# Kernel tuning notes

Hardware: AMD Instinct MI355X
Metric: run time of the kernel (lower is better)

## Reference

```python
import jax, jax.numpy as jnp
import numpy as np

N_NODES = 200000
N_EDGES = 600000
EMB = 128
HID = 128
N_RELS = 64
N_MOTIFS = 512
N_CENTERS = 256
N_NODE_CLASSES = 16


def _linear_params(key, out_dim, in_dim):
    kw, kb = jax.random.split(key)
    s = 1.0 / np.sqrt(in_dim)
    w = jax.random.uniform(kw, (out_dim, in_dim), jnp.float32, -s, s)
    b = jax.random.uniform(kb, (out_dim,), jnp.float32, -s, s)
    return w, b


def setup_inputs() -> dict:
    key = jax.random.key(0)
    ks = jax.random.split(key, 12)
    lin_w, lin_b = _linear_params(ks[2], HID, EMB)
    conv1_w, conv1_b = _linear_params(ks[3], HID, HID)
    conv2_w, conv2_b = _linear_params(ks[4], HID, HID)
    edge_w, edge_b = _linear_params(ks[5], N_RELS, 2 * HID)
    motif_w, motif_b = _linear_params(ks[6], N_MOTIFS, HID)
    node_w, node_b = _linear_params(ks[7], N_NODE_CLASSES, HID)
    return {
        "node_emb": jax.random.normal(ks[0], (N_NODES, EMB), jnp.float32),
        "rel_emb": jax.random.normal(ks[1], (N_RELS, EMB), jnp.float32),
        "lin_w": lin_w, "lin_b": lin_b,
        "conv1_w": conv1_w, "conv1_b": conv1_b,
        "conv2_w": conv2_w, "conv2_b": conv2_b,
        "edge_w": edge_w, "edge_b": edge_b,
        "motif_w": motif_w, "motif_b": motif_b,
        "node_w": node_w, "node_b": node_b,
        "node_ids": jnp.arange(N_NODES, dtype=jnp.int32),
        "rel_ids": jax.random.randint(ks[8], (N_EDGES,), 0, N_RELS, jnp.int32),
        "center_mol_idx": jax.random.randint(ks[9], (N_CENTERS,), 0, N_NODES, jnp.int32),
        "edge_index": jax.random.randint(ks[10], (2, N_EDGES), 0, N_NODES, jnp.int32),
    }


def _gine_conv(x, edge_index, edge_attr, w, b):
    # PyG GINEConv (eps=0): nn((1+eps)*x + sum_j relu(x_j + e_ji))
    src, dst = edge_index[0], edge_index[1]
    msg = jax.nn.relu(x[src] + edge_attr)               # [E, H]
    agg = jax.ops.segment_sum(msg, dst, num_segments=x.shape[0])  # [N, H]
    return (agg + x) @ w.T + b


def reference(node_emb, rel_emb, lin_w, lin_b, conv1_w, conv1_b,
              conv2_w, conv2_b, edge_w, edge_b, motif_w, motif_b,
              node_w, node_b, node_ids, rel_ids, center_mol_idx, edge_index):
    x = node_emb[node_ids]            # [N, EMB]
    edge_attr = rel_emb[rel_ids]      # [E, EMB]
    x = x @ lin_w.T + lin_b           # [N, H]
    edge_attr = edge_attr @ lin_w.T + lin_b  # [E, H]
    x = _gine_conv(x, edge_index, edge_attr, conv1_w, conv1_b)
    x = jax.nn.relu(x)
    x = _gine_conv(x, edge_index, edge_attr, conv2_w, conv2_b)
    edge_pred_input = jnp.concatenate([x[edge_index[0]], x[edge_index[1]]], axis=1)  # [E, 2H]
    edge_class = edge_pred_input @ edge_w.T + edge_b       # [E, num_rels]
    center = x[center_mol_idx]                             # [C, H]
    motif_pred = center @ motif_w.T + motif_b              # [C, num_motifs]
    node_class = x @ node_w.T + node_b                     # [N, 16]
    return (edge_class, motif_pred, node_class)
```

## Files before the change

kernel.cpp:

```cpp
#include <hip/hip_runtime.h>
#include <hip/hip_bf16.h>

#define N_NODES 200000
#define N_EDGES 600000
#define EMB 128
#define HID 128
#define N_RELS 64
#define N_MOTIFS 512
#define N_CENTERS 256
#define NCLS 16

#define SCAN_C 512
#define NB_SCAN ((N_NODES + SCAN_C - 1) / SCAN_C)

typedef unsigned short u16;
typedef __attribute__((ext_vector_type(8))) short short8;
typedef __attribute__((ext_vector_type(4))) float f32x4;

__device__ __forceinline__ float bf2f(u16 u) {
    unsigned int i = ((unsigned int)u) << 16;
    float f; __builtin_memcpy(&f, &i, 4); return f;
}
__device__ __forceinline__ u16 f2bf(float f) {
    unsigned int x; __builtin_memcpy(&x, &f, 4);
    x += 0x7fffu + ((x >> 16) & 1u);
    return (u16)(x >> 16);
}

#define O_LINW   0
#define O_LINB   16384
#define O_C1W    16512
#define O_C1B    32896
#define O_C2W    33024
#define O_C2B    49408
#define O_EW     49536
#define O_EB     65920
#define O_MW     65984
#define O_MB     131520
#define O_NW     132032
#define O_NB     134080
#define N_WB     134096

__global__ void k_cvt(const float* __restrict__ lw, const float* __restrict__ lb,
                      const float* __restrict__ c1w, const float* __restrict__ c1b,
                      const float* __restrict__ c2w, const float* __restrict__ c2b,
                      const float* __restrict__ ew, const float* __restrict__ eb,
                      const float* __restrict__ mw, const float* __restrict__ mb,
                      const float* __restrict__ nw, const float* __restrict__ nb,
                      u16* __restrict__ wb)
{
    const int t = blockIdx.x * 256 + threadIdx.x;
    if (t >= N_WB) return;
    float v;
    if      (t < O_LINB) v = lw[t - O_LINW];
    else if (t < O_C1W)  v = lb[t - O_LINB];
    else if (t < O_C1B)  v = c1w[t - O_C1W];
    else if (t < O_C2W)  v = c1b[t - O_C1B];
    else if (t < O_C2B)  v = c2w[t - O_C2W];
    else if (t < O_EW)   v = c2b[t - O_C2B];
    else if (t < O_EB)   v = ew[t - O_EW];
    else if (t < O_MW)   v = eb[t - O_EB];
    else if (t < O_MB)   v = mw[t - O_MW];
    else if (t < O_NW)   v = mb[t - O_MB];
    else if (t < O_NB)   v = nw[t - O_NW];
    else                 v = nb[t - O_NB];
    wb[t] = f2bf(v);
}

__global__ void k_rel(const float* __restrict__ rel_emb, const float* __restrict__ lw,
                      const float* __restrict__ lb, float* __restrict__ rel_lin)
{
    __shared__ float e[EMB];
    const int r = blockIdx.x, h = threadIdx.x;
    e[h] = rel_emb[r * EMB + h];
    __syncthreads();
    const float* wr = lw + (size_t)h * EMB;
    float acc = lb[h];
    #pragma unroll
    for (int k0 = 0; k0 < EMB; k0 += 4) {
        f32x4 wv = *(const f32x4*)(wr + k0);
        #pragma unroll
        for (int j = 0; j < 4; ++j) acc += e[k0 + j] * wv[j];
    }
    rel_lin[r * HID + h] = acc;
}

__global__ void k_hist(const int* __restrict__ dst, int* __restrict__ deg)
{
    const int e = blockIdx.x * 256 + threadIdx.x;
    if (e < N_EDGES) atomicAdd(&deg[dst[e]], 1);
}

__global__ void k_scan1(const int* __restrict__ deg, int* __restrict__ bsum)
{
    __shared__ int sd[256];
    const int t = threadIdx.x, base = blockIdx.x * SCAN_C;
    int v = 0;
    int i0 = base + t, i1 = base + 256 + t;
    if (i0 < N_NODES) v += deg[i0];
    if (i1 < N_NODES) v += deg[i1];
    sd[t] = v; __syncthreads();
    for (int s = 128; s > 0; s >>= 1) {
        if (t < s) sd[t] += sd[t + s];
        __syncthreads();
    }
    if (t == 0) bsum[blockIdx.x] = sd[0];
}

__global__ void k_scan2(int* __restrict__ bsum, int* __restrict__ row_ptr)
{
    __shared__ int sh[512];
    const int t = threadIdx.x;
    int v = (t < NB_SCAN) ? bsum[t] : 0;
    sh[t] = v;
    for (int off = 1; off < 512; off <<= 1) {
        __syncthreads();
        int a = (t >= off) ? sh[t - off] : 0;
        __syncthreads();
        sh[t] += a;
    }
    __syncthreads();
    if (t < NB_SCAN) bsum[t] = sh[t] - v;
    if (t == 511) row_ptr[N_NODES] = sh[511];
}

__global__ void k_scan3(const int* __restrict__ deg, const int* __restrict__ bsum,
                        int* __restrict__ row_ptr)
{
    __shared__ int sh[256];
    const int t = threadIdx.x, base = blockIdx.x * SCAN_C;
    const int i0 = base + 2 * t, i1 = i0 + 1;
    int d0 = (i0 < N_NODES) ? deg[i0] : 0;
    int d1 = (i1 < N_NODES) ? deg[i1] : 0;
    int p = d0 + d1;
    sh[t] = p;
    for (int off = 1; off < 256; off <<= 1) {
        __syncthreads();
        int a = (t >= off) ? sh[t - off] : 0;
        __syncthreads();
        sh[t] += a;
    }
    __syncthreads();
    const int off = bsum[blockIdx.x] + sh[t] - p;
    if (i0 < N_NODES) row_ptr[i0] = off;
    if (i1 < N_NODES) row_ptr[i1] = off + d0;
}

__global__ void k_fill(const int* __restrict__ src, const int* __restrict__ dst,
                       const int* __restrict__ rid, const int* __restrict__ row_ptr,
                       int* __restrict__ cur, int* __restrict__ srcrid)
{
    const int e = blockIdx.x * 256 + threadIdx.x;
    if (e >= N_EDGES) return;
    const int d = dst[e];
    const int pos = row_ptr[d] + atomicAdd(&cur[d], 1);
    srcrid[pos] = src[e] * 64 + rid[e];
}

__global__ __launch_bounds__(256) void k_lin(
    const float* __restrict__ emb, const int* __restrict__ ids,
    const u16* __restrict__ w, const u16* __restrict__ bias,
    u16* __restrict__ out)
{
    const int wid = threadIdx.x >> 6, lane = threadIdx.x & 63;
    const int r15 = lane & 15, kg = (lane >> 4) * 8;
    const int arow = blockIdx.x * 64 + wid * 16 + r15;
    const int srow = ids[arow];
    const float* ar = emb + (size_t)srow * EMB + kg;
    short8 a[4];
    #pragma unroll
    for (int kk = 0; kk < 4; ++kk) {
        f32x4 a0 = *(const f32x4*)(ar + kk * 32);
        f32x4 a1 = *(const f32x4*)(ar + kk * 32 + 4);
        short8 t;
        #pragma unroll
        for (int j = 0; j < 4; ++j) { t[j] = (short)f2bf(a0[j]); t[4 + j] = (short)f2bf(a1[j]); }
        a[kk] = t;
    }
    f32x4 acc[8];
    #pragma unroll
    for (int nb = 0; nb < 8; ++nb) acc[nb] = (f32x4){0.f, 0.f, 0.f, 0.f};
    #pragma unroll
    for (int nb = 0; nb < 8; ++nb) {
        const u16* wr = w + (size_t)(nb * 16 + r15) * EMB + kg;
        #pragma unroll
        for (int kk = 0; kk < 4; ++kk) {
            short8 bv = *(const short8*)(wr + kk * 32);
            acc[nb] = __builtin_amdgcn_mfma_f32_16x16x32_bf16(a[kk], bv, acc[nb], 0, 0, 0);
        }
    }
    const int ob = blockIdx.x * 64 + wid * 16 + (lane >> 4) * 4;
    #pragma unroll
    for (int nb = 0; nb < 8; ++nb) {
        const int col = nb * 16 + r15;
        const float bn = bf2f(bias[col]);
        #pragma unroll
        for (int r = 0; r < 4; ++r)
            out[(size_t)(ob + r) * HID + col] = f2bf(acc[nb][r] + bn);
    }
}

#define RLD 132
#define ALD 136
__global__ __launch_bounds__(256) void k_fuse(
    const u16* __restrict__ x, const float* __restrict__ rel_lin,
    const int* __restrict__ row_ptr, const int* __restrict__ srcrid,
    const u16* __restrict__ w, const u16* __restrict__ bias,
    u16* __restrict__ out, const int do_relu)
{
    __shared__ float rel[N_RELS * RLD];
    __shared__ u16 atile[64 * ALD];
    {
        const int rr = threadIdx.x >> 2, qq = (threadIdx.x & 3) * 32;
        #pragma unroll
        for (int c = 0; c < 32; c += 4) {
            f32x4 v = *(const f32x4*)(rel_lin + rr * HID + qq + c);
            *(f32x4*)(&rel[rr * RLD + qq + c]) = v;
        }
    }
    __syncthreads();

    const int nl = threadIdx.x >> 2;
    const int n = blockIdx.x * 64 + nl;
    const int q = (threadIdx.x & 3) * 32;
    const int pbeg = row_ptr[n], pend = row_ptr[n + 1];

    float acc[32];
    #pragma unroll
    for (int j = 0; j < 32; ++j) acc[j] = 0.f;

    for (int p = pbeg; p < pend; ++p) {
        const int v = srcrid[p];
        const int s = v >> 6, r = v & 63;
        const u16* xp = x + (size_t)s * HID + q;
        const float* rp = &rel[r * RLD + q];
        #pragma unroll
        for (int c = 0; c < 4; ++c) {
            short8 xv = *(const short8*)(xp + c * 8);
            #pragma unroll
            for (int j = 0; j < 8; ++j)
                acc[c * 8 + j] += fmaxf(bf2f((u16)xv[j]) + rp[c * 8 + j], 0.f);
        }
    }
    {
        const u16* xp = x + (size_t)n * HID + q;
        #pragma unroll
        for (int c = 0; c < 4; ++c) {
            short8 xv = *(const short8*)(xp + c * 8);
            short8 t;
            #pragma unroll
            for (int j = 0; j < 8; ++j) t[j] = (short)f2bf(acc[c * 8 + j] + bf2f((u16)xv[j]));
            *(short8*)(&atile[nl * ALD + q + c * 8]) = t;
        }
    }
    __syncthreads();

    const int wid = threadIdx.x >> 6, lane = threadIdx.x & 63;
    const int r15 = lane & 15, kg = (lane >> 4) * 8;
    const int lrow = wid * 16 + r15;
    short8 a[4];
    #pragma unroll
    for (int kk = 0; kk < 4; ++kk) a[kk] = *(const short8*)(&atile[lrow * ALD + kg + kk * 32]);
    f32x4 accm[8];
    #pragma unroll
    for (int nb = 0; nb < 8; ++nb) accm[nb] = (f32x4){0.f, 0.f, 0.f, 0.f};
    #pragma unroll
    for (int nb = 0; nb < 8; ++nb) {
        const u16* wr = w + (size_t)(nb * 16 + r15) * HID + kg;
        #pragma unroll
        for (int kk = 0; kk < 4; ++kk) {
            short8 bv = *(const short8*)(wr + kk * 32);
            accm[nb] = __builtin_amdgcn_mfma_f32_16x16x32_bf16(a[kk], bv, accm[nb], 0, 0, 0);
        }
    }
    const int ob = blockIdx.x * 64 + wid * 16 + (lane >> 4) * 4;
    #pragma unroll
    for (int nb = 0; nb < 8; ++nb) {
        const int col = nb * 16 + r15;
        const float bn = bf2f(bias[col]);
        #pragma unroll
        for (int r = 0; r < 4; ++r) {
            float v = accm[nb][r] + bn;
            if (do_relu) v = fmaxf(v, 0.f);
            out[(size_t)(ob + r) * HID + col] = f2bf(v);
        }
    }
}

__global__ __launch_bounds__(256) void k_heads(
    const u16* __restrict__ x2, const u16* __restrict__ ew,
    const u16* __restrict__ nw, const u16* __restrict__ nbias,
    float* __restrict__ y, float* __restrict__ node_out)
{
    const int wid = threadIdx.x >> 6, lane = threadIdx.x & 63;
    const int r15 = lane & 15, kg = (lane >> 4) * 8;
    const int arow = blockIdx.x * 64 + wid * 16 + r15;
    const u16* xr = x2 + (size_t)arow * HID + kg;
    short8 a[4];
    #pragma unroll
    for (int kk = 0; kk < 4; ++kk) a[kk] = *(const short8*)(xr + kk * 32);

    f32x4 accs[4], accd[4], accn;
    #pragma unroll
    for (int nb = 0; nb < 4; ++nb) {
        accs[nb] = (f32x4){0.f, 0.f, 0.f, 0.f};
        accd[nb] = (f32x4){0.f, 0.f, 0.f, 0.f};
    }
    accn = (f32x4){0.f, 0.f, 0.f, 0.f};

    #pragma unroll
    for (int nb = 0; nb < 4; ++nb) {
        const u16* wr = ew + (size_t)(nb * 16 + r15) * 256 + kg;
        #pragma unroll
        for (int kk = 0; kk < 4; ++kk) {
            short8 bs = *(const short8*)(wr + kk * 32);
            short8 bd = *(const short8*)(wr + 128 + kk * 32);
            accs[nb] = __builtin_amdgcn_mfma_f32_16x16x32_bf16(a[kk], bs, accs[nb], 0, 0, 0);
            accd[nb] = __builtin_amdgcn_mfma_f32_16x16x32_bf16(a[kk], bd, accd[nb], 0, 0, 0);
        }
    }
    {
        const u16* wr = nw + (size_t)r15 * HID + kg;
        #pragma unroll
        for (int kk = 0; kk < 4; ++kk) {
            short8 bv = *(const short8*)(wr + kk * 32);
            accn = __builtin_amdgcn_mfma_f32_16x16x32_bf16(a[kk], bv, accn, 0, 0, 0);
        }
    }

    const int ob = blockIdx.x * 64 + wid * 16 + (lane >> 4) * 4;
    #pragma unroll
    for (int nb = 0; nb < 4; ++nb) {
        const int col = nb * 16 + r15;
        #pragma unroll
        for (int r = 0; r < 4; ++r) {
            y[(size_t)(ob + r) * 128 + col] = accs[nb][r];
            y[(size_t)(ob + r) * 128 + 64 + col] = accd[nb][r];
        }
    }
    const float bn = bf2f(nbias[r15]);
    #pragma unroll
    for (int r = 0; r < 4; ++r)
        node_out[(size_t)(ob + r) * NCLS + r15] = accn[r] + bn;
}

__global__ __launch_bounds__(256) void k_eout(
    const float* __restrict__ y, const int* __restrict__ src, const int* __restrict__ dst,
    const float* __restrict__ eb, float* __restrict__ out)
{
    const int t = blockIdx.x * 256 + threadIdx.x;
    const int e = t >> 2;
    const int qq = (t & 3) * 16;
    const int s = src[e], d = dst[e];
    const float* ys = y + (size_t)s * 128 + qq;
    const float* yd = y + (size_t)d * 128 + 64 + qq;
    const float* ebp = eb + qq;
    float* op = out + (size_t)e * 64 + qq;
    #pragma unroll
    for (int c = 0; c < 4; ++c) {
        f32x4 vs = *(const f32x4*)(ys + c * 4);
        f32x4 vd = *(const f32x4*)(yd + c * 4);
        f32x4 vb = *(const f32x4*)(ebp + c * 4);
        f32x4 r;
        #pragma unroll
        for (int j = 0; j < 4; ++j) r[j] = vs[j] + vd[j] + vb[j];
        *(f32x4*)(op + c * 4) = r;
    }
}

__global__ void k_motif(const u16* __restrict__ x2, const int* __restrict__ centers,
                        const u16* __restrict__ mw, const u16* __restrict__ mb,
                        float* __restrict__ out)
{
    __shared__ float xs[HID];
    const int c = blockIdx.x, m = threadIdx.x;
    if (m < HID) xs[m] = bf2f(x2[(size_t)centers[c] * HID + m]);
    __syncthreads();
    const u16* wr = mw + (size_t)m * HID;
    float acc = bf2f(mb[m]);
    #pragma unroll
    for (int k0 = 0; k0 < HID; k0 += 8) {
        short8 wv = *(const short8*)(wr + k0);
        #pragma unroll
        for (int j = 0; j < 8; ++j) acc += xs[k0 + j] * bf2f((u16)wv[j]);
    }
    out[(size_t)c * N_MOTIFS + m] = acc;
}

extern "C" void kernel_launch(void* const* d_in, const int* in_sizes, int n_in,
                              void* d_out, int out_size, void* d_ws, size_t ws_size,
                              hipStream_t stream)
{
    const float* node_emb = (const float*)d_in[0];
    const float* rel_emb  = (const float*)d_in[1];
    const float* lin_w    = (const float*)d_in[2];
    const float* lin_b    = (const float*)d_in[3];
    const float* conv1_w  = (const float*)d_in[4];
    const float* conv1_b  = (const float*)d_in[5];
    const float* conv2_w  = (const float*)d_in[6];
    const float* conv2_b  = (const float*)d_in[7];
    const float* edge_w   = (const float*)d_in[8];
    const float* edge_b   = (const float*)d_in[9];
    const float* motif_w  = (const float*)d_in[10];
    const float* motif_b  = (const float*)d_in[11];
    const float* node_w   = (const float*)d_in[12];
    const float* node_b   = (const float*)d_in[13];
    const int* node_ids = (const int*)d_in[14];
    const int* rel_ids  = (const int*)d_in[15];
    const int* centers  = (const int*)d_in[16];
    const int* src      = (const int*)d_in[17];
    const int* dst      = ((const int*)d_in[17]) + N_EDGES;

    char* ws = (char*)d_ws;
    float* rel_lin = (float*)ws;
    u16*   wb      = (u16*)(ws + 32768);
    u16*   x0      = (u16*)(ws + 524288);
    u16*   x1      = (u16*)(ws + 524288 + 51200000);
    float* y       = (float*)(ws + 524288 + 2 * 51200000);
    char*  csr     = ws + 524288 + 2 * 51200000 + 102400000;
    int*   deg     = (int*)csr;
    int*   cur     = (int*)(csr + 800000);
    int*   row_ptr = (int*)(csr + 1600000);
    int*   srcrid  = (int*)(csr + 2400032);
    int*   bsum    = (int*)(csr + 4800032);
    u16*   x2      = x0;

    float* out_edge  = (float*)d_out;
    float* out_motif = out_edge + (size_t)N_EDGES * 64;
    float* out_node  = out_motif + (size_t)N_CENTERS * N_MOTIFS;

    k_cvt<<<(N_WB + 255) / 256, 256, 0, stream>>>(
        lin_w, lin_b, conv1_w, conv1_b, conv2_w, conv2_b,
        edge_w, edge_b, motif_w, motif_b, node_w, node_b, wb);
    hipMemsetAsync(deg, 0, 1600000, stream);
    k_rel<<<N_RELS, 128, 0, stream>>>(rel_emb, lin_w, lin_b, rel_lin);

    k_hist<<<(N_EDGES + 255) / 256, 256, 0, stream>>>(dst, deg);
    k_scan1<<<NB_SCAN, 256, 0, stream>>>(deg, bsum);
    k_scan2<<<1, 512, 0, stream>>>(bsum, row_ptr);
    k_scan3<<<NB_SCAN, 256, 0, stream>>>(deg, bsum, row_ptr);
    k_fill<<<(N_EDGES + 255) / 256, 256, 0, stream>>>(src, dst, rel_ids, row_ptr, cur, srcrid);

    k_lin<<<N_NODES / 64, 256, 0, stream>>>(node_emb, node_ids, wb + O_LINW, wb + O_LINB, x0);
    k_fuse<<<N_NODES / 64, 256, 0, stream>>>(x0, rel_lin, row_ptr, srcrid,
                                             wb + O_C1W, wb + O_C1B, x1, 1);
    k_fuse<<<N_NODES / 64, 256, 0, stream>>>(x1, rel_lin, row_ptr, srcrid,
                                             wb + O_C2W, wb + O_C2B, x2, 0);
    k_heads<<<N_NODES / 64, 256, 0, stream>>>(x2, wb + O_EW, wb + O_NW, wb + O_NB, y, out_node);
    k_eout<<<(N_EDGES * 4) / 256, 256, 0, stream>>>(y, src, dst, edge_b, out_edge);
    k_motif<<<N_CENTERS, N_MOTIFS, 0, stream>>>(x2, centers, wb + O_MW, wb + O_MB, out_motif);
}
```

Before: 508.0 us.

## Read rel table from global, unroll edge loop by two, store head projections as bf16

The GINE aggregation kernel no longer stages the 64x128 fp32 relation table in shared memory. It reads the table straight from global memory/L1 and handles two edges per iteration so more gathers are in flight at once. This frees about 33KB of LDS per block, which should allow more blocks per CU. The per-node src/dst projections y are now stored as bf16 instead of fp32, halving the bytes the edge-output kernel gathers, at the cost of extra rounding in the edge logits.

New measurement: 541.0 us. 1.06x slower.

```diff
diff --git a/kernel.cpp b/kernel.cpp
--- a/kernel.cpp
+++ b/kernel.cpp
@@ -200,7 +200,6 @@
     }
 }
 
-#define RLD 132
 #define ALD 136
 __global__ __launch_bounds__(256) void k_fuse(
     const u16* __restrict__ x, const float* __restrict__ rel_lin,
@@ -208,17 +207,7 @@
     const u16* __restrict__ w, const u16* __restrict__ bias,
     u16* __restrict__ out, const int do_relu)
 {
-    __shared__ float rel[N_RELS * RLD];
     __shared__ u16 atile[64 * ALD];
-    {
-        const int rr = threadIdx.x >> 2, qq = (threadIdx.x & 3) * 32;
-        #pragma unroll
-        for (int c = 0; c < 32; c += 4) {
-            f32x4 v = *(const f32x4*)(rel_lin + rr * HID + qq + c);
-            *(f32x4*)(&rel[rr * RLD + qq + c]) = v;
-        }
-    }
-    __syncthreads();
 
     const int nl = threadIdx.x >> 2;
     const int n = blockIdx.x * 64 + nl;
@@ -229,11 +218,36 @@
     #pragma unroll
     for (int j = 0; j < 32; ++j) acc[j] = 0.f;
 
-    for (int p = pbeg; p < pend; ++p) {
+    int p = pbeg;
+    for (; p + 2 <= pend; p += 2) {
+        const int v0 = srcrid[p], v1 = srcrid[p + 1];
+        const int s0 = v0 >> 6, r0 = v0 & 63;
+        const int s1 = v1 >> 6, r1 = v1 & 63;
+        const u16* xp0 = x + (size_t)s0 * HID + q;
+        const u16* xp1 = x + (size_t)s1 * HID + q;
+        const float* rp0 = rel_lin + r0 * HID + q;
+        const float* rp1 = rel_lin + r1 * HID + q;
+        short8 xv0[4], xv1[4];
+        f32x4 rv0[8], rv1[8];
+        #pragma unroll
+        for (int c = 0; c < 4; ++c) { xv0[c] = *(const short8*)(xp0 + c * 8);
+                                      xv1[c] = *(const short8*)(xp1 + c * 8); }
+        #pragma unroll
+        for (int c = 0; c < 8; ++c) { rv0[c] = *(const f32x4*)(rp0 + c * 4);
+                                      rv1[c] = *(const f32x4*)(rp1 + c * 4); }
+        #pragma unroll
+        for (int c = 0; c < 4; ++c)
+            #pragma unroll
+            for (int j = 0; j < 8; ++j) {
+                acc[c * 8 + j] += fmaxf(bf2f((u16)xv0[c][j]) + rv0[c * 2 + (j >> 2)][j & 3], 0.f);
+                acc[c * 8 + j] += fmaxf(bf2f((u16)xv1[c][j]) + rv1[c * 2 + (j >> 2)][j & 3], 0.f);
+            }
+    }
+    if (p < pend) {
         const int v = srcrid[p];
         const int s = v >> 6, r = v & 63;
         const u16* xp = x + (size_t)s * HID + q;
-        const float* rp = &rel[r * RLD + q];
+        const float* rp = rel_lin + r * HID + q;
         #pragma unroll
         for (int c = 0; c < 4; ++c) {
             short8 xv = *(const short8*)(xp + c * 8);
@@ -290,7 +304,7 @@
 __global__ __launch_bounds__(256) void k_heads(
     const u16* __restrict__ x2, const u16* __restrict__ ew,
     const u16* __restrict__ nw, const u16* __restrict__ nbias,
-    float* __restrict__ y, float* __restrict__ node_out)
+    u16* __restrict__ y, float* __restrict__ node_out)
 {
     const int wid = threadIdx.x >> 6, lane = threadIdx.x & 63;
     const int r15 = lane & 15, kg = (lane >> 4) * 8;
@@ -334,8 +348,8 @@
         const int col = nb * 16 + r15;
         #pragma unroll
         for (int r = 0; r < 4; ++r) {
-            y[(size_t)(ob + r) * 128 + col] = accs[nb][r];
-            y[(size_t)(ob + r) * 128 + 64 + col] = accd[nb][r];
+            y[(size_t)(ob + r) * 128 + col] = f2bf(accs[nb][r]);
+            y[(size_t)(ob + r) * 128 + 64 + col] = f2bf(accd[nb][r]);
         }
     }
     const float bn = bf2f(nbias[r15]);
@@ -345,26 +359,30 @@
 }
 
 __global__ __launch_bounds__(256) void k_eout(
-    const float* __restrict__ y, const int* __restrict__ src, const int* __restrict__ dst,
+    const u16* __restrict__ y, const int* __restrict__ src, const int* __restrict__ dst,
     const float* __restrict__ eb, float* __restrict__ out)
 {
     const int t = blockIdx.x * 256 + threadIdx.x;
     const int e = t >> 2;
     const int qq = (t & 3) * 16;
     const int s = src[e], d = dst[e];
-    const float* ys = y + (size_t)s * 128 + qq;
-    const float* yd = y + (size_t)d * 128 + 64 + qq;
+    const u16* ys = y + (size_t)s * 128 + qq;
+    const u16* yd = y + (size_t)d * 128 + 64 + qq;
     const float* ebp = eb + qq;
     float* op = out + (size_t)e * 64 + qq;
     #pragma unroll
-    for (int c = 0; c < 4; ++c) {
-        f32x4 vs = *(const f32x4*)(ys + c * 4);
-        f32x4 vd = *(const f32x4*)(yd + c * 4);
-        f32x4 vb = *(const f32x4*)(ebp + c * 4);
-        f32x4 r;
-        #pragma unroll
-        for (int j = 0; j < 4; ++j) r[j] = vs[j] + vd[j] + vb[j];
-        *(f32x4*)(op + c * 4) = r;
+    for (int c = 0; c < 2; ++c) {
+        short8 vs = *(const short8*)(ys + c * 8);
+        short8 vd = *(const short8*)(yd + c * 8);
+        #pragma unroll
+        for (int h = 0; h < 2; ++h) {
+            f32x4 vb = *(const f32x4*)(ebp + c * 8 + h * 4);
+            f32x4 r;
+            #pragma unroll
+            for (int j = 0; j < 4; ++j)
+                r[j] = bf2f((u16)vs[h * 4 + j]) + bf2f((u16)vd[h * 4 + j]) + vb[j];
+            *(f32x4*)(op + c * 8 + h * 4) = r;
+        }
     }
 }
 
@@ -416,7 +434,7 @@
     u16*   wb      = (u16*)(ws + 32768);
     u16*   x0      = (u16*)(ws + 524288);
     u16*   x1      = (u16*)(ws + 524288 + 51200000);
-    float* y       = (float*)(ws + 524288 + 2 * 51200000);
+    u16*   y       = (u16*)(ws + 524288 + 2 * 51200000);
     char*  csr     = ws + 524288 + 2 * 51200000 + 102400000;
     int*   deg     = (int*)csr;
     int*   cur     = (int*)(csr + 800000);
```
